# Optimization experiments

Hardware: AMD Instinct MI355X
Metric: run time of the kernel (lower is better)

Reference implementation:

```python
import jax, jax.numpy as jnp
import numpy as np

N_POINTS = 4000000
RESOLUTION = 512
HASHMAP_SIZE = 1 << 19  # 2**log2_hashmap_size
N_FEATURES = 4
# Instant-NGP style spatial-hash primes
PRIME_X = np.uint32(1)
PRIME_Y = np.uint32(2654435761)
PRIME_Z = np.uint32(805459861)


def setup_inputs() -> dict:
    key = jax.random.key(0)
    k1, k2 = jax.random.split(key)
    inputs = jax.random.randint(k1, (N_POINTS, 3), 0, RESOLUTION, dtype=jnp.int32)
    embeddings = jax.random.normal(k2, (HASHMAP_SIZE, N_FEATURES), dtype=jnp.float32)
    return {"inputs": inputs, "embeddings": embeddings,
            "resolution": RESOLUTION, "hashmap_size": HASHMAP_SIZE}


def _hash_index(coords_u32, hashmap_size):
    # coords_u32: [N,3] uint32; XOR-of-products spatial hash, modulo table size
    h = (coords_u32[:, 0] * PRIME_X) ^ (coords_u32[:, 1] * PRIME_Y) ^ (coords_u32[:, 2] * PRIME_Z)
    return (h % np.uint32(hashmap_size)).astype(jnp.int32)


def reference(inputs, embeddings, resolution, hashmap_size):
    # cnt_np_embed forward (axis='xy'):
    #   gather binarized (STE sign) embeddings by spatial hash of 3D int coords,
    #   scatter-count +1/-1 occurrences into a [scale, scale, F, 2] plane grid,
    #   then normalize to per-cell fractions (Bernoulli probabilities).
    scale = resolution - 2
    idx = _hash_index(inputs.astype(jnp.uint32), hashmap_size)      # [N]
    emb = embeddings[idx]                                           # [N, F] irregular gather
    # STE_binary forward: clamp then sign -> {-1, +1}
    b = jnp.where(emb >= 0, 1.0, -1.0).astype(emb.dtype)            # [N, F]
    pos = (1.0 + b) * 0.5                                           # 1 where +1
    neg = (1.0 - b) * 0.5                                           # 1 where -1
    # project onto the xy plane; clip coords into the (resolution-2)^2 grid
    u = jnp.clip(inputs[:, 0], 0, scale - 1)
    v = jnp.clip(inputs[:, 1], 0, scale - 1)
    cell = (u * scale + v).astype(jnp.int32)                        # [N]
    num_cells = scale * scale
    pn_pos = jax.ops.segment_sum(pos, cell, num_segments=num_cells)  # [S*S, F]
    pn_neg = jax.ops.segment_sum(neg, cell, num_segments=num_cells)  # [S*S, F]
    pn = jnp.stack([pn_pos, pn_neg], axis=-1).reshape(scale, scale, -1, 2)
    pn_sum = jnp.sum(pn, axis=-1, keepdims=True) + 1e-6
    return pn / pn_sum
```

## Files before the change

kernel.cpp:

```cpp
#include <hip/hip_runtime.h>

#define SCALE   510
#define NCELLS  (SCALE * SCALE)
#define NF      4
#define PRIME_Y 2654435761u
#define PRIME_Z 805459861u

#define NGRP    32
#define NBLKA   512
#define CAPA    320
#define PAT     1024
#define SEGASTR 321

#define NBKT    256
#define NBLKB   512
#define SUBS    16
#define CAPB    72
#define PBT     1024
#define LROWB   258

#define PHT     1024
#define SPILLCAP 65536

#define GSEGA_BYTES  ((size_t)NBLKA * NGRP * CAPA * 4)
#define RECS_BYTES   ((size_t)NBLKB * NBKT * CAPB * 2)
#define CNTA_BYTES   ((size_t)NGRP * NBLKA * 2)
#define CNTG_BYTES   ((size_t)NBKT * NBLKB * 2)
#define SIGN_BYTES   ((size_t)262144)
#define HDR_BYTES    ((size_t)256)
#define SPILLA_BYTES ((size_t)SPILLCAP * 8)
#define SPILLB_BYTES ((size_t)SPILLCAP * 4)

__global__ void signtab_kernel(const float4* __restrict__ emb,
                               unsigned char* __restrict__ signtab,
                               unsigned int* __restrict__ hdr,
                               unsigned int hsize) {
    unsigned int i = blockIdx.x * blockDim.x + threadIdx.x;
    if (i < 2) hdr[i] = 0;
    if (i * 2 >= hsize) return;
    float4 e0 = emb[2 * i + 0];
    float4 e1 = emb[2 * i + 1];
    unsigned int b = 0;
    if (e0.x >= 0.0f) b |= 1u << 0;
    if (e0.y >= 0.0f) b |= 1u << 1;
    if (e0.z >= 0.0f) b |= 1u << 2;
    if (e0.w >= 0.0f) b |= 1u << 3;
    if (e1.x >= 0.0f) b |= 1u << 4;
    if (e1.y >= 0.0f) b |= 1u << 5;
    if (e1.z >= 0.0f) b |= 1u << 6;
    if (e1.w >= 0.0f) b |= 1u << 7;
    signtab[i] = (unsigned char)b;
}

__device__ __forceinline__ void split_point(
        int x, int y, int z,
        unsigned int* __restrict__ segA, unsigned int* __restrict__ rankA,
        unsigned int* __restrict__ spillcnt, unsigned long long* __restrict__ spillA,
        unsigned int hmask) {
    unsigned int h = (unsigned int)x
                   ^ ((unsigned int)y * PRIME_Y)
                   ^ ((unsigned int)z * PRIME_Z);
    unsigned int idx = h & hmask;
    unsigned int g   = idx >> 14;
    unsigned int hl  = idx & 0x3FFFu;
    unsigned int u = (unsigned int)min(max(x, 0), SCALE - 1);
    unsigned int v = (unsigned int)min(max(y, 0), SCALE - 1);
    unsigned int w = (hl << 18) | (u << 9) | v;
    unsigned int r = atomicAdd(&rankA[g], 1u);
    if (r < CAPA) {
        segA[g * SEGASTR + r] = w;
    } else {
        unsigned int rs = atomicAdd(spillcnt, 1u);
        if (rs < SPILLCAP)
            spillA[rs] = ((unsigned long long)g << 32) | w;
    }
}

__global__ __launch_bounds__(PAT)
void hashsplit_kernel(const int* __restrict__ inputs,
                      unsigned int* __restrict__ gsegA,
                      unsigned short* __restrict__ cntA,
                      unsigned int* __restrict__ hdr,
                      unsigned long long* __restrict__ spillA,
                      int n, unsigned int hmask) {
    __shared__ unsigned int segA[NGRP * SEGASTR];
    __shared__ unsigned int rankA[NGRP];
    const int t = threadIdx.x, b = blockIdx.x;
    if (t < NGRP) rankA[t] = 0;
    __syncthreads();

    const int nquad = n >> 2;
    const int qpb = (nquad + NBLKA - 1) / NBLKA;
    const int q0 = b * qpb;
    const int q1 = min(q0 + qpb, nquad);
    const int4* in4 = (const int4*)inputs;
    for (int q = q0 + t; q < q1; q += PAT) {
        int4 A = in4[3 * q + 0];
        int4 B = in4[3 * q + 1];
        int4 C = in4[3 * q + 2];
        split_point(A.x, A.y, A.z, segA, rankA, hdr, spillA, hmask);
        split_point(A.w, B.x, B.y, segA, rankA, hdr, spillA, hmask);
        split_point(B.z, B.w, C.x, segA, rankA, hdr, spillA, hmask);
        split_point(C.y, C.z, C.w, segA, rankA, hdr, spillA, hmask);
    }
    if (b == 0 && t == 0) {
        for (int p = nquad * 4; p < n; ++p)
            split_point(inputs[3 * p], inputs[3 * p + 1], inputs[3 * p + 2],
                        segA, rankA, hdr, spillA, hmask);
    }
    __syncthreads();

    for (int j = t; j < NGRP * CAPA; j += PAT)
        gsegA[(size_t)b * NGRP * CAPA + j] =
            segA[(j / CAPA) * SEGASTR + (j % CAPA)];
    if (t < NGRP)
        cntA[t * NBLKA + b] = (unsigned short)min(rankA[t], (unsigned int)CAPA);
}

__device__ __forceinline__ void proc_rec(
        unsigned int w,
        const unsigned int* __restrict__ slice,
        unsigned short* __restrict__ segB, unsigned int* __restrict__ rankB,
        unsigned int* __restrict__ spillcntB, unsigned int* __restrict__ spillB) {
    unsigned int hl = w >> 18;
    unsigned int u  = (w >> 9) & 0x1FFu;
    unsigned int v  = w & 0x1FFu;
    unsigned int nib = (slice[hl >> 3] >> ((hl & 7u) * 4u)) & 0xFu;
    unsigned int bkt = u >> 1;
    unsigned int rec = ((u & 1u) << 13) | (v << 4) | nib;
    unsigned int r = atomicAdd(&rankB[bkt], 1u);
    if (r < CAPB) {
        segB[r * LROWB + bkt] = (unsigned short)rec;
    } else {
        unsigned int rs = atomicAdd(spillcntB, 1u);
        if (rs < SPILLCAP) spillB[rs] = (bkt << 16) | rec;
    }
}

__global__ __launch_bounds__(PBT)
void binlookup_kernel(const unsigned int* __restrict__ gsegA,
                      const unsigned short* __restrict__ cntA,
                      const unsigned int* __restrict__ sig32,
                      unsigned short* __restrict__ recs,
                      unsigned short* __restrict__ cntg,
                      const unsigned int* __restrict__ hdr,
                      const unsigned long long* __restrict__ spillA,
                      unsigned int* __restrict__ spillcntB,
                      unsigned int* __restrict__ spillB) {
    __shared__ unsigned int   slice[2048];
    __shared__ unsigned short segB[CAPB * LROWB];
    __shared__ unsigned int   rankB[NBKT];
    __shared__ unsigned short cA[32];
    const int t = threadIdx.x, b = blockIdx.x;
    const int g = b / SUBS, k = b % SUBS;
    if (t < NBKT) rankB[t] = 0;
    if (t < 32)  cA[t] = cntA[g * NBLKA + k * 32 + t];
    for (int i = t; i < 2048; i += PBT) slice[i] = sig32[g * 2048 + i];
    __syncthreads();

    for (int j = t; j < 32 * CAPA; j += PBT) {
        const int s = j / CAPA, r = j % CAPA;
        if (r < (int)cA[s]) {
            unsigned int w = gsegA[((size_t)(k * 32 + s) * NGRP + g) * CAPA + r];
            proc_rec(w, slice, segB, rankB, spillcntB, spillB);
        }
    }
    if (k == 0) {
        unsigned int ns = min(hdr[0], (unsigned int)SPILLCAP);
        for (unsigned int i2 = t; i2 < ns; i2 += PBT) {
            unsigned long long e = spillA[i2];
            if ((unsigned int)(e >> 32) == (unsigned int)g)
                proc_rec((unsigned int)e, slice, segB, rankB, spillcntB, spillB);
        }
    }
    __syncthreads();

    unsigned int* gout = (unsigned int*)(recs + (size_t)b * NBKT * CAPB);
    for (int j = t; j < NBKT * CAPB / 2; j += PBT) {
        const int bkt = j / (CAPB / 2);
        const int r   = (j % (CAPB / 2)) * 2;
        unsigned int lo = segB[r * LROWB + bkt];
        unsigned int hi = segB[(r + 1) * LROWB + bkt];
        gout[j] = lo | (hi << 16);
    }
    if (t < NBKT)
        cntg[t * NBLKB + b] = (unsigned short)min(rankB[t], (unsigned int)CAPB);
}

__device__ __forceinline__ void hist_add(unsigned long long* hist,
                                         unsigned int rec) {
    unsigned int nib = rec & 0xFu;
    unsigned int v   = (rec >> 4) & 0x1FFu;
    unsigned int ul  = rec >> 13;
    unsigned long long add = 1ull
        | ((unsigned long long)(nib & 1u)        << 12)
        | ((unsigned long long)((nib >> 1) & 1u) << 24)
        | ((unsigned long long)((nib >> 2) & 1u) << 36)
        | ((unsigned long long)((nib >> 3) & 1u) << 48);
    atomicAdd(&hist[ul * SCALE + v], add);
}

__global__ __launch_bounds__(PHT)
void histnorm_kernel(const unsigned short* __restrict__ recs,
                     const unsigned short* __restrict__ cntg,
                     const unsigned int* __restrict__ hdr,
                     const unsigned int* __restrict__ spillB,
                     float* __restrict__ out) {
    __shared__ unsigned long long hist[2 * SCALE];
    __shared__ unsigned short cl[NBLKB];
    const int t = threadIdx.x, b = blockIdx.x;
    for (int i = t; i < 2 * SCALE; i += PHT) hist[i] = 0;
    if (t < NBLKB) cl[t] = cntg[b * NBLKB + t];
    __syncthreads();

    for (int j = t; j < NBLKB * CAPB / 2; j += PHT) {
        const int s  = j / (CAPB / 2);
        const int wi = j % (CAPB / 2);
        const unsigned int* segp = (const unsigned int*)
            (recs + ((size_t)s * NBKT + b) * CAPB);
        unsigned int w = segp[wi];
        const int c = cl[s], r0 = wi * 2;
        if (r0 < c)     hist_add(hist, w & 0xFFFFu);
        if (r0 + 1 < c) hist_add(hist, w >> 16);
    }
    const unsigned int ns = min(hdr[1], (unsigned int)SPILLCAP);
    for (unsigned int i2 = t; i2 < ns; i2 += PHT) {
        unsigned int w = spillB[i2];
        if ((int)(w >> 16) == b) hist_add(hist, w & 0xFFFFu);
    }
    __syncthreads();

    const size_t outbase = (size_t)(2 * b) * SCALE * 8;
    for (int c = t; c < 2 * SCALE; c += PHT) {
        unsigned long long vv = hist[c];
        float cc = (float)(unsigned int)(vv & 0xFFFull);
        float p0 = (float)(unsigned int)((vv >> 12) & 0xFFFull);
        float p1 = (float)(unsigned int)((vv >> 24) & 0xFFFull);
        float p2 = (float)(unsigned int)((vv >> 36) & 0xFFFull);
        float p3 = (float)(unsigned int)((vv >> 48) & 0xFFFull);
        float inv = 1.0f / (cc + 1e-6f);
        float4 o0, o1;
        o0.x = p0 * inv; o0.y = (cc - p0) * inv;
        o0.z = p1 * inv; o0.w = (cc - p1) * inv;
        o1.x = p2 * inv; o1.y = (cc - p2) * inv;
        o1.z = p3 * inv; o1.w = (cc - p3) * inv;
        float4* op = (float4*)(out + outbase + (size_t)c * 8);
        op[0] = o0;
        op[1] = o1;
    }
}

__global__ void scatter_fb_kernel(const int* __restrict__ inputs,
                                  const float4* __restrict__ emb,
                                  unsigned long long* __restrict__ cnt,
                                  int n, unsigned int hmask) {
    int i = blockIdx.x * blockDim.x + threadIdx.x;
    if (i >= n) return;
    int x = inputs[3 * i], y = inputs[3 * i + 1], z = inputs[3 * i + 2];
    unsigned int h = (unsigned int)x ^ ((unsigned int)y * PRIME_Y)
                   ^ ((unsigned int)z * PRIME_Z);
    float4 e = emb[h & hmask];
    unsigned long long add = 1ull;
    if (e.x >= 0.0f) add |= 1ull << 12;
    if (e.y >= 0.0f) add |= 1ull << 24;
    if (e.z >= 0.0f) add |= 1ull << 36;
    if (e.w >= 0.0f) add |= 1ull << 48;
    int u = min(max(x, 0), SCALE - 1);
    int v = min(max(y, 0), SCALE - 1);
    atomicAdd(&cnt[u * SCALE + v], add);
}

__global__ void normalize_fb_kernel(const unsigned long long* __restrict__ cnt,
                                    float* __restrict__ out) {
    int i = blockIdx.x * blockDim.x + threadIdx.x;
    if (i >= NCELLS) return;
    unsigned long long v = cnt[i];
    float c  = (float)(unsigned int)(v & 0xFFFull);
    float p0 = (float)(unsigned int)((v >> 12) & 0xFFFull);
    float p1 = (float)(unsigned int)((v >> 24) & 0xFFFull);
    float p2 = (float)(unsigned int)((v >> 36) & 0xFFFull);
    float p3 = (float)(unsigned int)((v >> 48) & 0xFFFull);
    float inv = 1.0f / (c + 1e-6f);
    float4 o0, o1;
    o0.x = p0 * inv; o0.y = (c - p0) * inv;
    o0.z = p1 * inv; o0.w = (c - p1) * inv;
    o1.x = p2 * inv; o1.y = (c - p2) * inv;
    o1.z = p3 * inv; o1.w = (c - p3) * inv;
    float4* outv = (float4*)(out + (size_t)i * 8);
    outv[0] = o0; outv[1] = o1;
}

extern "C" void kernel_launch(void* const* d_in, const int* in_sizes, int n_in,
                              void* d_out, int out_size, void* d_ws, size_t ws_size,
                              hipStream_t stream) {
    const int*    inputs = (const int*)d_in[0];
    const float4* emb    = (const float4*)d_in[1];
    int n = in_sizes[0] / 3;
    unsigned int hsize = (unsigned int)(in_sizes[1] / NF);
    unsigned int hmask = hsize - 1;

    const size_t need = GSEGA_BYTES + RECS_BYTES + CNTA_BYTES + CNTG_BYTES
                      + SIGN_BYTES + HDR_BYTES + SPILLA_BYTES + SPILLB_BYTES;

    if (ws_size >= need && hsize == (1u << 19)) {
        char* w = (char*)d_ws;
        unsigned int*       gsegA   = (unsigned int*)w;            w += GSEGA_BYTES;
        unsigned short*     recs    = (unsigned short*)w;          w += RECS_BYTES;
        unsigned short*     cntA    = (unsigned short*)w;          w += CNTA_BYTES;
        unsigned short*     cntg    = (unsigned short*)w;          w += CNTG_BYTES;
        unsigned char*      signtab = (unsigned char*)w;           w += SIGN_BYTES;
        unsigned int*       hdr     = (unsigned int*)w;            w += HDR_BYTES;
        unsigned long long* spillA  = (unsigned long long*)w;      w += SPILLA_BYTES;
        unsigned int*       spillB  = (unsigned int*)w;

        signtab_kernel<<<((int)(hsize / 2) + 255) / 256, 256, 0, stream>>>(
            emb, signtab, hdr, hsize);
        hashsplit_kernel<<<NBLKA, PAT, 0, stream>>>(
            inputs, gsegA, cntA, hdr, spillA, n, hmask);
        binlookup_kernel<<<NBLKB, PBT, 0, stream>>>(
            gsegA, cntA, (const unsigned int*)signtab, recs, cntg,
            hdr, spillA, hdr + 1, spillB);
        histnorm_kernel<<<255, PHT, 0, stream>>>(
            recs, cntg, hdr, spillB, (float*)d_out);
    } else {
        unsigned long long* cnt = (unsigned long long*)d_ws;
        hipMemsetAsync(cnt, 0, (size_t)NCELLS * 8, stream);
        const int threads = 256;
        scatter_fb_kernel<<<(n + threads - 1) / threads, threads, 0, stream>>>(
            inputs, emb, cnt, n, hmask);
        normalize_fb_kernel<<<(NCELLS + threads - 1) / threads, threads, 0, stream>>>(
            cnt, (float*)d_out);
    }
}
```

Before: 44.75 us.

## Fuse sign-table build into hash split kernel and regroup hash buckets

The separate sign-table kernel is folded into the hash-split launch as extra blocks, and the header counters are reset with a memset instead. The hash space is split into 64 groups of 8K entries instead of 32 groups of 16K, with matching capacity and sub-block changes so each lookup block loads a smaller shared sign slice. The split loop is also unrolled twice to keep more loads in flight. This removes one launch and shrinks shared memory per block, but adds a memset launch and changes overflow behaviour for the smaller per-group capacities.

```diff
diff --git a/kernel.cpp b/kernel.cpp
--- a/kernel.cpp
+++ b/kernel.cpp
@@ -6,16 +6,17 @@
 #define PRIME_Y 2654435761u
 #define PRIME_Z 805459861u
 
-#define NGRP    32
+#define NGRP    64
 #define NBLKA   512
-#define CAPA    320
+#define CAPA    176
+#define SEGASTR 177
 #define PAT     1024
-#define SEGASTR 321
+#define SIGBLKS 256
 
 #define NBKT    256
 #define NBLKB   512
-#define SUBS    16
-#define CAPB    72
+#define SUBS    8
+#define CAPB    64
 #define PBT     1024
 #define LROWB   258
 
@@ -30,27 +31,6 @@
 #define HDR_BYTES    ((size_t)256)
 #define SPILLA_BYTES ((size_t)SPILLCAP * 8)
 #define SPILLB_BYTES ((size_t)SPILLCAP * 4)
-
-__global__ void signtab_kernel(const float4* __restrict__ emb,
-                               unsigned char* __restrict__ signtab,
-                               unsigned int* __restrict__ hdr,
-                               unsigned int hsize) {
-    unsigned int i = blockIdx.x * blockDim.x + threadIdx.x;
-    if (i < 2) hdr[i] = 0;
-    if (i * 2 >= hsize) return;
-    float4 e0 = emb[2 * i + 0];
-    float4 e1 = emb[2 * i + 1];
-    unsigned int b = 0;
-    if (e0.x >= 0.0f) b |= 1u << 0;
-    if (e0.y >= 0.0f) b |= 1u << 1;
-    if (e0.z >= 0.0f) b |= 1u << 2;
-    if (e0.w >= 0.0f) b |= 1u << 3;
-    if (e1.x >= 0.0f) b |= 1u << 4;
-    if (e1.y >= 0.0f) b |= 1u << 5;
-    if (e1.z >= 0.0f) b |= 1u << 6;
-    if (e1.w >= 0.0f) b |= 1u << 7;
-    signtab[i] = (unsigned char)b;
-}
 
 __device__ __forceinline__ void split_point(
         int x, int y, int z,
@@ -61,8 +41,8 @@
                    ^ ((unsigned int)y * PRIME_Y)
                    ^ ((unsigned int)z * PRIME_Z);
     unsigned int idx = h & hmask;
-    unsigned int g   = idx >> 14;
-    unsigned int hl  = idx & 0x3FFFu;
+    unsigned int g   = idx >> 13;
+    unsigned int hl  = idx & 0x1FFFu;
     unsigned int u = (unsigned int)min(max(x, 0), SCALE - 1);
     unsigned int v = (unsigned int)min(max(y, 0), SCALE - 1);
     unsigned int w = (hl << 18) | (u << 9) | v;
@@ -78,14 +58,34 @@
 
 __global__ __launch_bounds__(PAT)
 void hashsplit_kernel(const int* __restrict__ inputs,
+                      const float4* __restrict__ emb,
                       unsigned int* __restrict__ gsegA,
                       unsigned short* __restrict__ cntA,
+                      unsigned char* __restrict__ signtab,
                       unsigned int* __restrict__ hdr,
                       unsigned long long* __restrict__ spillA,
                       int n, unsigned int hmask) {
     __shared__ unsigned int segA[NGRP * SEGASTR];
     __shared__ unsigned int rankA[NGRP];
     const int t = threadIdx.x, b = blockIdx.x;
+
+    if (b >= NBLKA) {
+        unsigned int i = (unsigned int)(b - NBLKA) * PAT + t;
+        float4 e0 = emb[2 * i + 0];
+        float4 e1 = emb[2 * i + 1];
+        unsigned int bb = 0;
+        if (e0.x >= 0.0f) bb |= 1u << 0;
+        if (e0.y >= 0.0f) bb |= 1u << 1;
+        if (e0.z >= 0.0f) bb |= 1u << 2;
+        if (e0.w >= 0.0f) bb |= 1u << 3;
+        if (e1.x >= 0.0f) bb |= 1u << 4;
+        if (e1.y >= 0.0f) bb |= 1u << 5;
+        if (e1.z >= 0.0f) bb |= 1u << 6;
+        if (e1.w >= 0.0f) bb |= 1u << 7;
+        signtab[i] = (unsigned char)bb;
+        return;
+    }
+
     if (t < NGRP) rankA[t] = 0;
     __syncthreads();
 
@@ -94,14 +94,32 @@
     const int q0 = b * qpb;
     const int q1 = min(q0 + qpb, nquad);
     const int4* in4 = (const int4*)inputs;
-    for (int q = q0 + t; q < q1; q += PAT) {
-        int4 A = in4[3 * q + 0];
-        int4 B = in4[3 * q + 1];
-        int4 C = in4[3 * q + 2];
-        split_point(A.x, A.y, A.z, segA, rankA, hdr, spillA, hmask);
-        split_point(A.w, B.x, B.y, segA, rankA, hdr, spillA, hmask);
-        split_point(B.z, B.w, C.x, segA, rankA, hdr, spillA, hmask);
-        split_point(C.y, C.z, C.w, segA, rankA, hdr, spillA, hmask);
+    int q = q0 + t;
+    for (; q + PAT < q1; q += 2 * PAT) {
+        int4 A0 = in4[3 * q + 0];
+        int4 B0 = in4[3 * q + 1];
+        int4 C0 = in4[3 * q + 2];
+        int q2 = q + PAT;
+        int4 A1 = in4[3 * q2 + 0];
+        int4 B1 = in4[3 * q2 + 1];
+        int4 C1 = in4[3 * q2 + 2];
+        split_point(A0.x, A0.y, A0.z, segA, rankA, hdr, spillA, hmask);
+        split_point(A0.w, B0.x, B0.y, segA, rankA, hdr, spillA, hmask);
+        split_point(B0.z, B0.w, C0.x, segA, rankA, hdr, spillA, hmask);
+        split_point(C0.y, C0.z, C0.w, segA, rankA, hdr, spillA, hmask);
+        split_point(A1.x, A1.y, A1.z, segA, rankA, hdr, spillA, hmask);
+        split_point(A1.w, B1.x, B1.y, segA, rankA, hdr, spillA, hmask);
+        split_point(B1.z, B1.w, C1.x, segA, rankA, hdr, spillA, hmask);
+        split_point(C1.y, C1.z, C1.w, segA, rankA, hdr, spillA, hmask);
+    }
+    for (; q < q1; q += PAT) {
+        int4 A0 = in4[3 * q + 0];
+        int4 B0 = in4[3 * q + 1];
+        int4 C0 = in4[3 * q + 2];
+        split_point(A0.x, A0.y, A0.z, segA, rankA, hdr, spillA, hmask);
+        split_point(A0.w, B0.x, B0.y, segA, rankA, hdr, spillA, hmask);
+        split_point(B0.z, B0.w, C0.x, segA, rankA, hdr, spillA, hmask);
+        split_point(C0.y, C0.z, C0.w, segA, rankA, hdr, spillA, hmask);
     }
     if (b == 0 && t == 0) {
         for (int p = nquad * 4; p < n; ++p)
@@ -147,21 +165,21 @@
                       const unsigned long long* __restrict__ spillA,
                       unsigned int* __restrict__ spillcntB,
                       unsigned int* __restrict__ spillB) {
-    __shared__ unsigned int   slice[2048];
+    __shared__ unsigned int   slice[1024];
     __shared__ unsigned short segB[CAPB * LROWB];
     __shared__ unsigned int   rankB[NBKT];
-    __shared__ unsigned short cA[32];
+    __shared__ unsigned short cA[NGRP];
     const int t = threadIdx.x, b = blockIdx.x;
-    const int g = b / SUBS, k = b % SUBS;
+    const int g = b >> 3, k = b & (SUBS - 1);
     if (t < NBKT) rankB[t] = 0;
-    if (t < 32)  cA[t] = cntA[g * NBLKA + k * 32 + t];
-    for (int i = t; i < 2048; i += PBT) slice[i] = sig32[g * 2048 + i];
-    __syncthreads();
-
-    for (int j = t; j < 32 * CAPA; j += PBT) {
+    if (t < NGRP) cA[t] = cntA[g * NBLKA + k * NGRP + t];
+    if (t < 1024) slice[t] = sig32[g * 1024 + t];
+    __syncthreads();
+
+    for (int j = t; j < NGRP * CAPA; j += PBT) {
         const int s = j / CAPA, r = j % CAPA;
         if (r < (int)cA[s]) {
-            unsigned int w = gsegA[((size_t)(k * 32 + s) * NGRP + g) * CAPA + r];
+            unsigned int w = gsegA[((size_t)(k * NGRP + s) * NGRP + g) * CAPA + r];
             proc_rec(w, slice, segB, rankB, spillcntB, spillB);
         }
     }
@@ -177,8 +195,8 @@
 
     unsigned int* gout = (unsigned int*)(recs + (size_t)b * NBKT * CAPB);
     for (int j = t; j < NBKT * CAPB / 2; j += PBT) {
-        const int bkt = j / (CAPB / 2);
-        const int r   = (j % (CAPB / 2)) * 2;
+        const int bkt = j >> 5;
+        const int r   = (j & 31) * 2;
         unsigned int lo = segB[r * LROWB + bkt];
         unsigned int hi = segB[(r + 1) * LROWB + bkt];
         gout[j] = lo | (hi << 16);
@@ -214,8 +232,8 @@
     __syncthreads();
 
     for (int j = t; j < NBLKB * CAPB / 2; j += PHT) {
-        const int s  = j / (CAPB / 2);
-        const int wi = j % (CAPB / 2);
+        const int s  = j >> 5;
+        const int wi = j & 31;
         const unsigned int* segp = (const unsigned int*)
             (recs + ((size_t)s * NBKT + b) * CAPB);
         unsigned int w = segp[wi];
@@ -313,10 +331,9 @@
         unsigned long long* spillA  = (unsigned long long*)w;      w += SPILLA_BYTES;
         unsigned int*       spillB  = (unsigned int*)w;
 
-        signtab_kernel<<<((int)(hsize / 2) + 255) / 256, 256, 0, stream>>>(
-            emb, signtab, hdr, hsize);
-        hashsplit_kernel<<<NBLKA, PAT, 0, stream>>>(
-            inputs, gsegA, cntA, hdr, spillA, n, hmask);
+        hipMemsetAsync(hdr, 0, 8, stream);
+        hashsplit_kernel<<<NBLKA + SIGBLKS, PAT, 0, stream>>>(
+            inputs, emb, gsegA, cntA, signtab, hdr, spillA, n, hmask);
         binlookup_kernel<<<NBLKB, PBT, 0, stream>>>(
             gsegA, cntA, (const unsigned int*)signtab, recs, cntg,
             hdr, spillA, hdr + 1, spillB);
```

After: 52.40 us. +17.1%, slower.

## Merge sign-table build into hashsplit and skip writing unused bucket slots

Applied to the files above, without the earlier changes.

The separate sign-table kernel is folded into the hashsplit launch as 256 extra blocks, and the header counters are reset with a memset. Hashsplit and binlookup now copy only the occupied part of each bucket (rounded up to 16 words) to global memory instead of the full capacity. Histnorm reads only those rounded-up ranges. This cuts a kernel launch and a good share of intermediate traffic, at the cost of an extra memset node, an extra barrier, and some more per-thread branching.

```diff
diff --git a/kernel.cpp b/kernel.cpp
--- a/kernel.cpp
+++ b/kernel.cpp
@@ -9,8 +9,9 @@
 #define NGRP    32
 #define NBLKA   512
 #define CAPA    320
+#define SEGASTR 321
 #define PAT     1024
-#define SEGASTR 321
+#define SIGBLKS 256
 
 #define NBKT    256
 #define NBLKB   512
@@ -30,27 +31,6 @@
 #define HDR_BYTES    ((size_t)256)
 #define SPILLA_BYTES ((size_t)SPILLCAP * 8)
 #define SPILLB_BYTES ((size_t)SPILLCAP * 4)
-
-__global__ void signtab_kernel(const float4* __restrict__ emb,
-                               unsigned char* __restrict__ signtab,
-                               unsigned int* __restrict__ hdr,
-                               unsigned int hsize) {
-    unsigned int i = blockIdx.x * blockDim.x + threadIdx.x;
-    if (i < 2) hdr[i] = 0;
-    if (i * 2 >= hsize) return;
-    float4 e0 = emb[2 * i + 0];
-    float4 e1 = emb[2 * i + 1];
-    unsigned int b = 0;
-    if (e0.x >= 0.0f) b |= 1u << 0;
-    if (e0.y >= 0.0f) b |= 1u << 1;
-    if (e0.z >= 0.0f) b |= 1u << 2;
-    if (e0.w >= 0.0f) b |= 1u << 3;
-    if (e1.x >= 0.0f) b |= 1u << 4;
-    if (e1.y >= 0.0f) b |= 1u << 5;
-    if (e1.z >= 0.0f) b |= 1u << 6;
-    if (e1.w >= 0.0f) b |= 1u << 7;
-    signtab[i] = (unsigned char)b;
-}
 
 __device__ __forceinline__ void split_point(
         int x, int y, int z,
@@ -78,14 +58,36 @@
 
 __global__ __launch_bounds__(PAT)
 void hashsplit_kernel(const int* __restrict__ inputs,
+                      const float4* __restrict__ emb,
                       unsigned int* __restrict__ gsegA,
                       unsigned short* __restrict__ cntA,
+                      unsigned char* __restrict__ signtab,
                       unsigned int* __restrict__ hdr,
                       unsigned long long* __restrict__ spillA,
                       int n, unsigned int hmask) {
-    __shared__ unsigned int segA[NGRP * SEGASTR];
-    __shared__ unsigned int rankA[NGRP];
-    const int t = threadIdx.x, b = blockIdx.x;
+    __shared__ unsigned int   segA[NGRP * SEGASTR];
+    __shared__ unsigned int   rankA[NGRP];
+    __shared__ unsigned short cwA[NGRP];
+    const int t = threadIdx.x, b0 = blockIdx.x;
+
+    if (b0 < SIGBLKS) {
+        unsigned int i = (unsigned int)b0 * PAT + t;
+        float4 e0 = emb[2 * i + 0];
+        float4 e1 = emb[2 * i + 1];
+        unsigned int bb = 0;
+        if (e0.x >= 0.0f) bb |= 1u << 0;
+        if (e0.y >= 0.0f) bb |= 1u << 1;
+        if (e0.z >= 0.0f) bb |= 1u << 2;
+        if (e0.w >= 0.0f) bb |= 1u << 3;
+        if (e1.x >= 0.0f) bb |= 1u << 4;
+        if (e1.y >= 0.0f) bb |= 1u << 5;
+        if (e1.z >= 0.0f) bb |= 1u << 6;
+        if (e1.w >= 0.0f) bb |= 1u << 7;
+        signtab[i] = (unsigned char)bb;
+        return;
+    }
+    const int b = b0 - SIGBLKS;
+
     if (t < NGRP) rankA[t] = 0;
     __syncthreads();
 
@@ -110,11 +112,18 @@
     }
     __syncthreads();
 
-    for (int j = t; j < NGRP * CAPA; j += PAT)
-        gsegA[(size_t)b * NGRP * CAPA + j] =
-            segA[(j / CAPA) * SEGASTR + (j % CAPA)];
-    if (t < NGRP)
-        cntA[t * NBLKA + b] = (unsigned short)min(rankA[t], (unsigned int)CAPA);
+    if (t < NGRP) {
+        unsigned int c = min(rankA[t], (unsigned int)CAPA);
+        cntA[t * NBLKA + b] = (unsigned short)c;
+        cwA[t] = (unsigned short)min((c + 15u) & ~15u, (unsigned int)CAPA);
+    }
+    __syncthreads();
+
+    for (int j = t; j < NGRP * CAPA; j += PAT) {
+        const int g = j / CAPA, r = j % CAPA;
+        if (r < (int)cwA[g])
+            gsegA[(size_t)b * NGRP * CAPA + j] = segA[g * SEGASTR + r];
+    }
 }
 
 __device__ __forceinline__ void proc_rec(
@@ -151,6 +160,7 @@
     __shared__ unsigned short segB[CAPB * LROWB];
     __shared__ unsigned int   rankB[NBKT];
     __shared__ unsigned short cA[32];
+    __shared__ unsigned short wlim[NBKT];
     const int t = threadIdx.x, b = blockIdx.x;
     const int g = b / SUBS, k = b % SUBS;
     if (t < NBKT) rankB[t] = 0;
@@ -175,16 +185,25 @@
     }
     __syncthreads();
 
+    if (t < NBKT) {
+        unsigned int c = min(rankB[t], (unsigned int)CAPB);
+        cntg[t * NBLKB + b] = (unsigned short)c;
+        wlim[t] = (unsigned short)min(((c + 31u) >> 5) << 4,
+                                      (unsigned int)(CAPB / 2));
+    }
+    __syncthreads();
+
     unsigned int* gout = (unsigned int*)(recs + (size_t)b * NBKT * CAPB);
     for (int j = t; j < NBKT * CAPB / 2; j += PBT) {
         const int bkt = j / (CAPB / 2);
-        const int r   = (j % (CAPB / 2)) * 2;
-        unsigned int lo = segB[r * LROWB + bkt];
-        unsigned int hi = segB[(r + 1) * LROWB + bkt];
-        gout[j] = lo | (hi << 16);
-    }
-    if (t < NBKT)
-        cntg[t * NBLKB + b] = (unsigned short)min(rankB[t], (unsigned int)CAPB);
+        const int wi  = j % (CAPB / 2);
+        if (wi < (int)wlim[bkt]) {
+            const int r = wi * 2;
+            unsigned int lo = segB[r * LROWB + bkt];
+            unsigned int hi = segB[(r + 1) * LROWB + bkt];
+            gout[j] = lo | (hi << 16);
+        }
+    }
 }
 
 __device__ __forceinline__ void hist_add(unsigned long long* hist,
@@ -216,12 +235,16 @@
     for (int j = t; j < NBLKB * CAPB / 2; j += PHT) {
         const int s  = j / (CAPB / 2);
         const int wi = j % (CAPB / 2);
-        const unsigned int* segp = (const unsigned int*)
-            (recs + ((size_t)s * NBKT + b) * CAPB);
-        unsigned int w = segp[wi];
-        const int c = cl[s], r0 = wi * 2;
-        if (r0 < c)     hist_add(hist, w & 0xFFFFu);
-        if (r0 + 1 < c) hist_add(hist, w >> 16);
+        const int c  = cl[s];
+        const int wl = min(((c + 31) >> 5) << 4, CAPB / 2);
+        if (wi < wl) {
+            const unsigned int* segp = (const unsigned int*)
+                (recs + ((size_t)s * NBKT + b) * CAPB);
+            unsigned int w = segp[wi];
+            const int r0 = wi * 2;
+            if (r0 < c)     hist_add(hist, w & 0xFFFFu);
+            if (r0 + 1 < c) hist_add(hist, w >> 16);
+        }
     }
     const unsigned int ns = min(hdr[1], (unsigned int)SPILLCAP);
     for (unsigned int i2 = t; i2 < ns; i2 += PHT) {
@@ -313,10 +336,9 @@
         unsigned long long* spillA  = (unsigned long long*)w;      w += SPILLA_BYTES;
         unsigned int*       spillB  = (unsigned int*)w;
 
-        signtab_kernel<<<((int)(hsize / 2) + 255) / 256, 256, 0, stream>>>(
-            emb, signtab, hdr, hsize);
-        hashsplit_kernel<<<NBLKA, PAT, 0, stream>>>(
-            inputs, gsegA, cntA, hdr, spillA, n, hmask);
+        hipMemsetAsync(hdr, 0, 8, stream);
+        hashsplit_kernel<<<SIGBLKS + NBLKA, PAT, 0, stream>>>(
+            inputs, emb, gsegA, cntA, signtab, hdr, spillA, n, hmask);
         binlookup_kernel<<<NBLKB, PBT, 0, stream>>>(
             gsegA, cntA, (const unsigned int*)signtab, recs, cntg,
             hdr, spillA, hdr + 1, spillB);
```

New measurement: 47.84 us. +6.9%, slower.
